# Kernel tuning notes

Measured on AMD Instinct MI355X. Metric: run time of the kernel, lower is better.

Reference implementation:

```python
import jax, jax.numpy as jnp
import numpy as np

N_QUBITS = 7
N_LAYERS = 2
DIM = 2 ** N_QUBITS  # 128
NORM_FACTOR = 1.0


def _cnot_gather_idx(n):
    # CNOT chain (0,1),(1,2),...,(n-2,n-1) plus wraparound (n-1,0).
    # new_state[x] = old_state[idx[x]]; apply gates in reverse to arange.
    gates = [(i, i + 1) for i in range(n - 1)] + [(n - 1, 0)]
    idx = np.arange(2 ** n)
    for c, t in reversed(gates):
        cbit = 1 << (n - 1 - c)  # pennylane wire 0 = most significant bit
        tbit = 1 << (n - 1 - t)
        idx = np.where((idx & cbit) > 0, idx ^ tbit, idx)
    return jnp.asarray(idx)

CNOT_IDX = _cnot_gather_idx(N_QUBITS)


def silu(x):
    return x * jax.nn.sigmoid(x)


def cayley(A_real, A_imag):
    # Hermitianize then Cayley transform -> unitary, per layer. [L,D,D]
    A = A_real.astype(jnp.complex64) + 1j * A_imag.astype(jnp.complex64)
    A = A + jnp.conj(jnp.swapaxes(A, -1, -2))
    I = jnp.eye(DIM, dtype=A.dtype)
    return jnp.matmul(A - 1j * I, jnp.linalg.inv(A + 1j * I))


def _single_qubit_gate(theta_x, theta_y):
    # combined G = RY(theta_y) @ RX(theta_x) applied to every qubit
    cx, sx = jnp.cos(theta_x / 2), jnp.sin(theta_x / 2)
    cy, sy = jnp.cos(theta_y / 2), jnp.sin(theta_y / 2)
    RX = jnp.stack([jnp.stack([cx + 0j, -1j * sx]), jnp.stack([-1j * sx, cx + 0j])])
    RY = jnp.stack([jnp.stack([cy + 0j, -sy + 0j]), jnp.stack([sy + 0j, cy + 0j])])
    return RY @ RX


def quantum_evolve(psi, coeffs, q_mats):
    # psi: [N, DIM] complex64 normalized state vectors
    N = psi.shape[0]
    for j in range(N_LAYERS):
        psi = psi @ q_mats[j].T  # QubitUnitary: new = U @ old
        G = _single_qubit_gate(coeffs[j, 0], coeffs[j, 1])
        psi = psi.reshape((N,) + (2,) * N_QUBITS)
        for ax in range(1, N_QUBITS + 1):
            psi = jnp.moveaxis(jnp.tensordot(G, psi, axes=((1,), (ax,))), 0, ax)
        psi = psi.reshape(N, DIM)
        psi = psi[:, CNOT_IDX]  # CNOT chain is a fixed basis permutation
    return psi


def setup_inputs() -> dict:
    key = jax.random.key(0)
    ks = jax.random.split(key, 16)
    N, E = 50000, 800000
    in_nf, hid, out_nf = 128, 128, 128
    h = jax.random.normal(ks[0], (N, in_nf), dtype=jnp.float32)
    edge_index = jax.random.randint(ks[1], (2, E), 0, N)
    s = 0.05
    W_e1 = jax.random.normal(ks[2], (2 * in_nf, hid), dtype=jnp.float32) * s
    b_e1 = jnp.zeros((hid,), dtype=jnp.float32)
    W_e2 = jax.random.normal(ks[3], (hid, hid), dtype=jnp.float32) * s
    b_e2 = jnp.zeros((hid,), dtype=jnp.float32)
    W_enc = jax.random.normal(ks[4], (hid + in_nf, DIM), dtype=jnp.float32) * s
    b_enc = jnp.zeros((DIM,), dtype=jnp.float32)
    coeffs = jax.random.normal(ks[5], (N_LAYERS, 2), dtype=jnp.float32) * 0.1
    A_real = jax.random.normal(ks[6], (N_LAYERS, DIM, DIM), dtype=jnp.float32) * 0.01
    A_imag = jax.random.normal(ks[7], (N_LAYERS, DIM, DIM), dtype=jnp.float32) * 0.01
    W_dec = jax.random.normal(ks[8], (DIM, out_nf), dtype=jnp.float32) * s
    b_dec = jnp.zeros((out_nf,), dtype=jnp.float32)
    return {"h": h, "edge_index": edge_index, "W_e1": W_e1, "b_e1": b_e1,
            "W_e2": W_e2, "b_e2": b_e2, "W_enc": W_enc, "b_enc": b_enc,
            "coeffs": coeffs, "A_real": A_real, "A_imag": A_imag,
            "W_dec": W_dec, "b_dec": b_dec}


def reference(h, edge_index, W_e1, b_e1, W_e2, b_e2, W_enc, b_enc,
              coeffs, A_real, A_imag, W_dec, b_dec):
    row, col = edge_index[0], edge_index[1]
    # edge model: mij = MLP([h_src, h_tgt])
    e = jnp.concatenate([h[row], h[col]], axis=1)  # [E, 2*in_nf]
    e = silu(e @ W_e1 + b_e1)
    edge_feat = silu(e @ W_e2 + b_e2)  # [E, hid]
    # node model: scatter-sum aggregation over destination `row`
    agg = jax.ops.segment_sum(edge_feat, row, num_segments=h.shape[0]) / NORM_FACTOR
    q_input = jnp.concatenate([h, agg], axis=1) @ W_enc + b_enc  # [N, DIM]
    norm = jnp.sqrt(jnp.sum(q_input ** 2, axis=1, keepdims=True) + 1e-12)
    psi = (q_input / norm).astype(jnp.complex64)
    q_mats = cayley(A_real, A_imag)  # [L, DIM, DIM] unitary
    psi = quantum_evolve(psi, coeffs, q_mats)
    out = h + (jnp.real(psi) @ W_dec + b_dec)
    return out, edge_feat
```

## Files before the change

### kernel.cpp

```cpp
#include <hip/hip_runtime.h>
#include <math.h>

#define N_NODES 50000
#define N_EDGES 800000

typedef __attribute__((ext_vector_type(8))) short bf16x8;
typedef __attribute__((ext_vector_type(4))) short bf16x4;
typedef __attribute__((ext_vector_type(2))) short shortx2;
typedef __attribute__((ext_vector_type(4))) float f32x4;

__device__ __forceinline__ float silu_f(float x) {
    float d = 1.0f + __expf(-x);
    return x * __builtin_amdgcn_rcpf(d);
}

__device__ __forceinline__ unsigned short f2bf(float x) {
    union { float f; unsigned u; } v; v.f = x;
    unsigned r = v.u + 0x7FFFu + ((v.u >> 16) & 1u);
    return (unsigned short)(r >> 16);
}

__device__ __forceinline__ void atomic_pk_add_bf16(short* addr, shortx2 v) {
    typedef shortx2 __attribute__((address_space(1)))* gp1;
    __builtin_amdgcn_global_atomic_fadd_v2bf16((gp1)(unsigned long long)addr, v);
}

__global__ __launch_bounds__(256) void prep_kernel(const float* __restrict__ h,
                                                   short* __restrict__ hbf,
                                                   const int* __restrict__ ei,
                                                   int* __restrict__ cnt,
                                                   const float* __restrict__ A_real,
                                                   const float* __restrict__ A_imag,
                                                   float* __restrict__ H,
                                                   float* __restrict__ X) {
    const int bid = blockIdx.x;
    const int t = threadIdx.x;
    if (bid < 3125) {
        int i = bid * 256 + t;
        const float4* h4 = (const float4*)h;
        float4 v0 = h4[i * 2], v1 = h4[i * 2 + 1];
        bf16x8 b;
        b[0] = (short)f2bf(v0.x); b[1] = (short)f2bf(v0.y);
        b[2] = (short)f2bf(v0.z); b[3] = (short)f2bf(v0.w);
        b[4] = (short)f2bf(v1.x); b[5] = (short)f2bf(v1.y);
        b[6] = (short)f2bf(v1.z); b[7] = (short)f2bf(v1.w);
        ((bf16x8*)hbf)[i] = b;
        atomicAdd(&cnt[ei[i]], 1);
    } else {
        int p = bid - 3125;
        int L = p >> 2, q4 = p & 3;
        const float* ar = A_real + L * 16384;
        const float* ai = A_imag + L * 16384;
        float* hre = H + L * 32768;
        float* him = hre + 16384;
        float* xre = X + L * 32768;
        float* xim = xre + 16384;
        for (int m = 0; m < 16; ++m) {
            int idx = q4 * 4096 + t + 256 * m;
            int i = idx >> 7, j = idx & 127;
            float hr = ar[idx] + ar[j * 128 + i];
            float hi = ai[idx] - ai[j * 128 + i];
            hre[idx] = hr;
            him[idx] = hi;
            xre[idx] = hr;
            xim[idx] = hi - (i == j ? 1.0f : 0.0f);
        }
    }
}

__device__ __forceinline__ void ns_t_body(int blk, int t,
                                          const float* __restrict__ H,
                                          const float* __restrict__ X,
                                          float* __restrict__ T) {
    const int L = blk >> 4;
    const int i = (blk & 15) * 8 + (t >> 7);
    const int j = t & 127;
    const float* hre = H + L * 32768;
    const float* him = hre + 16384;
    const float* xre = X + L * 32768;
    const float* xim = xre + 16384;
    float accr = 0.f, acci = 0.f;
    #pragma unroll 4
    for (int k = 0; k < 128; ++k) {
        float hr = hre[i * 128 + k], hi = him[i * 128 + k];
        float xr = xre[k * 128 + j], xi = xim[k * 128 + j];
        accr += hr * xr - hi * xi;
        acci += hr * xi + hi * xr;
    }
    T[L * 32768 + i * 128 + j]          = accr - xim[i * 128 + j];
    T[L * 32768 + 16384 + i * 128 + j]  = acci + xre[i * 128 + j];
}

__device__ __forceinline__ void ns_x_body(int blk, int t,
                                          const float* __restrict__ X,
                                          const float* __restrict__ T,
                                          float* __restrict__ Xout) {
    const int L = blk >> 4;
    const int i = (blk & 15) * 8 + (t >> 7);
    const int j = t & 127;
    const float* xre = X + L * 32768;
    const float* xim = xre + 16384;
    const float* tre = T + L * 32768;
    const float* tim = tre + 16384;
    float accr = 0.f, acci = 0.f;
    #pragma unroll 4
    for (int k = 0; k < 128; ++k) {
        float xr = xre[i * 128 + k], xi = xim[i * 128 + k];
        float tr = tre[k * 128 + j], ti = tim[k * 128 + j];
        accr += xr * tr - xi * ti;
        acci += xr * ti + xi * tr;
    }
    Xout[L * 32768 + i * 128 + j]          = 2.0f * xre[i * 128 + j] - accr;
    Xout[L * 32768 + 16384 + i * 128 + j]  = 2.0f * xim[i * 128 + j] - acci;
}

__global__ __launch_bounds__(1024) void nst_scan_kernel(const float* __restrict__ H,
                                                        const float* __restrict__ X,
                                                        float* __restrict__ T,
                                                        const int* __restrict__ cnt,
                                                        int* __restrict__ cursor) {
    const int bid = blockIdx.x;
    const int t = threadIdx.x;
    if (bid < 32) { ns_t_body(bid, t, H, X, T); return; }
    __shared__ int sA[1024];
    __shared__ int sB[1024];
    const int CH = 49;
    int s = 0;
    #pragma unroll 4
    for (int i = 0; i < CH; ++i) {
        int idx = t * CH + i;
        if (idx < N_NODES) s += cnt[idx];
    }
    sA[t] = s;
    __syncthreads();
    int* src = sA;
    int* dst = sB;
    for (int off = 1; off < 1024; off <<= 1) {
        int v = src[t];
        if (t >= off) v += src[t - off];
        dst[t] = v;
        __syncthreads();
        int* tmp = src; src = dst; dst = tmp;
    }
    int run = (t == 0) ? 0 : src[t - 1];
    for (int i = 0; i < CH; ++i) {
        int idx = t * CH + i;
        if (idx < N_NODES) {
            cursor[idx] = run;
            run += cnt[idx];
        }
    }
}

__global__ __launch_bounds__(1024) void fill_nsx_kernel(const int* __restrict__ ei,
                                                        int* __restrict__ cursor,
                                                        int* __restrict__ elist,
                                                        const float* __restrict__ X,
                                                        const float* __restrict__ T,
                                                        float* __restrict__ Xout) {
    const int bid = blockIdx.x;
    const int t = threadIdx.x;
    if (bid < 782) {
        int e = bid * 1024 + t;
        if (e < N_EDGES) {
            int slot = atomicAdd(&cursor[ei[e]], 1);
            elist[slot] = e;
        }
        return;
    }
    ns_x_body(bid - 782, t, X, T, Xout);
}

__global__ __launch_bounds__(1024) void ns_t_kernel(const float* __restrict__ H,
                                                    const float* __restrict__ X,
                                                    float* __restrict__ T) {
    ns_t_body(blockIdx.x, threadIdx.x, H, X, T);
}

__global__ __launch_bounds__(1024) void ns_x_kernel(const float* __restrict__ X,
                                                    const float* __restrict__ T,
                                                    float* __restrict__ Xout) {
    ns_x_body(blockIdx.x, threadIdx.x, X, T, Xout);
}

__global__ __launch_bounds__(1024) void gateperm_kernel(const float* __restrict__ X,
                                                        const float* __restrict__ coeffs,
                                                        float* __restrict__ Y) {
    __shared__ float Mre[128 * 129];
    __shared__ float Mim[128 * 129];
    const int L = blockIdx.x;
    const int t = threadIdx.x;
    const float* xre = X + L * 32768;
    const float* xim = xre + 16384;

    for (int q = 0; q < 16; ++q) {
        int idx = t + 1024 * q;
        int i = idx >> 7, j = idx & 127;
        Mre[i * 129 + j] = (i == j ? 1.0f : 0.0f) + 2.0f * xim[idx];
        Mim[i * 129 + j] = -2.0f * xre[idx];
    }
    __syncthreads();

    const float tx = coeffs[2 * L + 0] * 0.5f;
    const float ty = coeffs[2 * L + 1] * 0.5f;
    const float cx = cosf(tx), sx = sinf(tx), cy = cosf(ty), sy = sinf(ty);
    const float G00r = cx * cy, G00i = sx * sy;
    const float G01r = -cx * sy, G01i = -sx * cy;
    const float G10r = cx * sy, G10i = -sx * cy;
    const float G11r = cx * cy, G11i = -sx * sy;

    for (int st = 0; st < 7; ++st) {
        int b = 1 << st;
        #pragma unroll
        for (int p = 0; p < 8; ++p) {
            int pid = t + 1024 * p;
            int col = pid & 127, ph = pid >> 7;
            int i0 = ((ph >> st) << (st + 1)) | (ph & (b - 1));
            int i1 = i0 | b;
            float v0r = Mre[i0 * 129 + col], v0i = Mim[i0 * 129 + col];
            float v1r = Mre[i1 * 129 + col], v1i = Mim[i1 * 129 + col];
            Mre[i0 * 129 + col] = G00r * v0r - G00i * v0i + G01r * v1r - G01i * v1i;
            Mim[i0 * 129 + col] = G00r * v0i + G00i * v0r + G01r * v1i + G01i * v1r;
            Mre[i1 * 129 + col] = G10r * v0r - G10i * v0i + G11r * v1r - G11i * v1i;
            Mim[i1 * 129 + col] = G10r * v0i + G10i * v0r + G11r * v1i + G11i * v1r;
        }
        __syncthreads();
    }

    const int cs[7] = {6, 5, 4, 3, 2, 1, 0};
    const int ts[7] = {0, 6, 5, 4, 3, 2, 1};
    float* yre = Y + L * 32768;
    float* yim = yre + 16384;
    for (int q = 0; q < 16; ++q) {
        int idx = t + 1024 * q;
        int ii_ = idx >> 7, col = idx & 127;
        int s = ii_;
        #pragma unroll
        for (int m = 0; m < 7; ++m) {
            int cbit = 1 << (6 - cs[m]);
            int tbit = 1 << (6 - ts[m]);
            if (s & cbit) s ^= tbit;
        }
        yre[idx] = Mre[s * 129 + col];
        yim[idx] = Mim[s * 129 + col];
    }
}

__global__ __launch_bounds__(512) void combine1_kernel(const float* __restrict__ Y,
                                                       float* __restrict__ ReM) {
    __shared__ float q1r[16384];
    __shared__ float q1i[16384];
    const int t = threadIdx.x;
    const float* q1re = Y;
    const float* q1im = Y + 16384;
    const float* q2re = Y + 32768;
    const float* q2im = Y + 49152;
    for (int q = 0; q < 32; ++q) {
        q1r[t + 512 * q] = q1re[t + 512 * q];
        q1i[t + 512 * q] = q1im[t + 512 * q];
    }
    __syncthreads();
    int i = blockIdx.x * 4 + (t >> 7);
    int j = t & 127;
    float acc = 0.f;
    for (int k = 0; k < 128; ++k) {
        acc += q2re[i * 128 + k] * q1r[k * 128 + j] - q2im[i * 128 + k] * q1i[k * 128 + j];
    }
    ReM[i * 128 + j] = acc;
}

__global__ __launch_bounds__(512) void combine2_kernel(const float* __restrict__ ReM,
                                                       const float* __restrict__ W_dec,
                                                       short* __restrict__ Dt) {
    __shared__ float ml[16384];
    __shared__ float wl[16384];
    const int t = threadIdx.x;
    for (int q = 0; q < 32; ++q) {
        ml[t + 512 * q] = ReM[t + 512 * q];
        wl[t + 512 * q] = W_dec[t + 512 * q];
    }
    __syncthreads();
    int k = blockIdx.x * 4 + (t >> 7);
    int j = t & 127;
    float acc = 0.f;
    for (int i = 0; i < 128; ++i) {
        acc += ml[i * 128 + k] * wl[i * 128 + j];
    }
    Dt[j * 128 + k] = (short)f2bf(acc);
}

__global__ __launch_bounds__(768)
__attribute__((amdgpu_waves_per_eu(3, 3)))
void edge_kernel(const short* __restrict__ hbf,
                 const int* __restrict__ ei,
                 const int* __restrict__ elist,
                 const float* __restrict__ W_e1,
                 const float* __restrict__ b_e1,
                 const float* __restrict__ W_e2,
                 const float* __restrict__ b_e2,
                 float* __restrict__ ef_out,
                 short* __restrict__ agg_bf) {
    __shared__ short w1f[64 * 64 * 8];
    __shared__ short w2f[32 * 64 * 8];
    __shared__ short c1s[12][16 * 68];

    const int t = threadIdx.x;
    const int lane = t & 63;
    const int w = t >> 6;
    const int l15 = lane & 15;
    const int kg = lane >> 4;

    {
        const float4* w1_4 = (const float4*)W_e1;
        for (int idx4 = t; idx4 < 8192; idx4 += 768) {
            int k = idx4 >> 5, j4 = idx4 & 31;
            float4 v = w1_4[idx4];
            int s = k >> 5, kgs = (k >> 3) & 3, e = k & 7;
            int fb = s * 8;
            float vz[4] = {v.x, v.y, v.z, v.w};
            #pragma unroll
            for (int z = 0; z < 4; ++z) {
                int j = j4 * 4 + z;
                int nf = j >> 4, jl = j & 15;
                w1f[((fb + nf) * 64 + kgs * 16 + jl) * 8 + e] = (short)f2bf(vz[z]);
            }
        }
        const float4* w2_4 = (const float4*)W_e2;
        for (int idx4 = t; idx4 < 4096; idx4 += 768) {
            int k = idx4 >> 5, j4 = idx4 & 31;
            float4 v = w2_4[idx4];
            int s2 = k >> 5, kgs = (k >> 3) & 3, e = k & 7;
            int fb = s2 * 8;
            float vz[4] = {v.x, v.y, v.z, v.w};
            #pragma unroll
            for (int z = 0; z < 4; ++z) {
                int j = j4 * 4 + z;
                int nf = j >> 4, jl = j & 15;
                w2f[((fb + nf) * 64 + kgs * 16 + jl) * 8 + e] = (short)f2bf(vz[z]);
            }
        }
    }
    float b1v[8], b2v[8];
    #pragma unroll
    for (int nf = 0; nf < 8; ++nf) {
        b1v[nf] = b_e1[nf * 16 + l15];
        b2v[nf] = b_e2[nf * 16 + l15];
    }
    __syncthreads();

    const bf16x8* hb8 = (const bf16x8*)hbf;
    const bf16x8* w1v = (const bf16x8*)w1f;
    const bf16x8* w2v = (const bf16x8*)w2f;
    short* myc1 = &c1s[w][0];
    const int nt = N_EDGES / 16;
    const int TW = gridDim.x * 12;
    const int wvid = blockIdx.x * 12 + w;
    int tile = (int)(((long long)nt * wvid) / TW);
    const int tend = (int)(((long long)nt * (wvid + 1)) / TW);
    if (tile >= tend) return;

    int el = elist[tile * 16 + l15];
    int ri = ei[el];
    int ci = ei[N_EDGES + el];
    bf16x8 a1[8];
    #pragma unroll
    for (int s = 0; s < 4; ++s) a1[s] = hb8[(size_t)ri * 16 + s * 4 + kg];
    #pragma unroll
    for (int s = 0; s < 4; ++s) a1[4 + s] = hb8[(size_t)ci * 16 + s * 4 + kg];

    bool hn = (tile + 1 < tend);
    int eln = 0, rin = 0, cin = 0;
    if (hn) {
        eln = elist[(tile + 1) * 16 + l15];
        rin = ei[eln];
        cin = ei[N_EDGES + eln];
    }

    float runsum[8];
    #pragma unroll
    for (int nf = 0; nf < 8; ++nf) runsum[nf] = 0.f;

    for (;;) {
        bool hn2 = (tile + 2 < tend);
        int eln2 = 0, rin2 = 0, cin2 = 0;
        if (hn2) {
            eln2 = elist[(tile + 2) * 16 + l15];
            rin2 = ei[eln2];
            cin2 = ei[N_EDGES + eln2];
        }

        f32x4 acc[8];
        #pragma unroll
        for (int nf = 0; nf < 8; ++nf) acc[nf] = (f32x4){0.f, 0.f, 0.f, 0.f};
        #pragma unroll
        for (int s = 0; s < 8; ++s) {
            #pragma unroll
            for (int nf = 0; nf < 8; ++nf) {
                bf16x8 b = w1v[(s * 8 + nf) * 64 + lane];
                acc[nf] = __builtin_amdgcn_mfma_f32_16x16x32_bf16(a1[s], b, acc[nf], 0, 0, 0);
            }
        }

        bf16x8 a1n[8];
        if (hn) {
            #pragma unroll
            for (int s = 0; s < 4; ++s) a1n[s] = hb8[(size_t)rin * 16 + s * 4 + kg];
            #pragma unroll
            for (int s = 0; s < 4; ++s) a1n[4 + s] = hb8[(size_t)cin * 16 + s * 4 + kg];
        }

        f32x4 acc2[8];
        #pragma unroll
        for (int nf = 0; nf < 8; ++nf) acc2[nf] = (f32x4){0.f, 0.f, 0.f, 0.f};
        #pragma unroll
        for (int half = 0; half < 2; ++half) {
            #pragma unroll
            for (int nfh = 0; nfh < 4; ++nfh) {
                int nf = half * 4 + nfh;
                #pragma unroll
                for (int r = 0; r < 4; ++r) {
                    int row = kg * 4 + r;
                    int c = nfh * 16 + l15;
                    myc1[row * 68 + c] = (short)f2bf(silu_f(acc[nf][r] + b1v[nf]));
                }
            }
            #pragma unroll
            for (int s2l = 0; s2l < 2; ++s2l) {
                int k0h = s2l * 32 + kg * 8;
                int base = l15 * 68 + k0h;
                bf16x4 lo = *(const bf16x4*)&myc1[base];
                bf16x4 hi = *(const bf16x4*)&myc1[base + 4];
                bf16x8 a2;
                #pragma unroll
                for (int z = 0; z < 4; ++z) { a2[z] = lo[z]; a2[4 + z] = hi[z]; }
                int s2 = half * 2 + s2l;
                #pragma unroll
                for (int nf = 0; nf < 8; ++nf) {
                    bf16x8 b = w2v[(s2 * 8 + nf) * 64 + lane];
                    acc2[nf] = __builtin_amdgcn_mfma_f32_16x16x32_bf16(a2, b, acc2[nf], 0, 0, 0);
                }
            }
        }

        int rw[4], ew[4];
        #pragma unroll
        for (int r = 0; r < 4; ++r) {
            rw[r] = __shfl(ri, kg * 4 + r);
            ew[r] = __shfl(el, kg * 4 + r);
        }
        int rwn0 = hn ? __shfl(rin, kg * 4) : -1;
        #pragma unroll
        for (int r = 0; r < 4; ++r) {
            float* efp = ef_out + (size_t)ew[r] * 128;
            #pragma unroll
            for (int nf = 0; nf < 8; ++nf) {
                int col = nf * 16 + l15;
                float v = silu_f(acc2[nf][r] + b2v[nf]);
                __builtin_nontemporal_store(v, efp + col);
                runsum[nf] += v;
            }
            bool end = (r < 3) ? (rw[r + 1] != rw[r]) : (rw[3] != rwn0);
            if (end) {
                short* agp = agg_bf + (size_t)rw[r] * 128;
                #pragma unroll
                for (int nf = 0; nf < 8; ++nf) {
                    float vn = __shfl_xor(runsum[nf], 1);
                    if ((l15 & 1) == 0) {
                        shortx2 pk;
                        pk.x = (short)f2bf(runsum[nf]);
                        pk.y = (short)f2bf(vn);
                        atomic_pk_add_bf16(agp + nf * 16 + l15, pk);
                    }
                    runsum[nf] = 0.f;
                }
            }
        }

        if (!hn) break;
        tile += 1;
        el = eln; ri = rin; ci = cin;
        #pragma unroll
        for (int s = 0; s < 8; ++s) a1[s] = a1n[s];
        hn = hn2; eln = eln2; rin = rin2; cin = cin2;
    }
}

__global__ __launch_bounds__(1024)
__attribute__((amdgpu_waves_per_eu(4, 4)))
void node_kernel(const short* __restrict__ hbf,
                 const short* __restrict__ agg_bf,
                 const float* __restrict__ W_enc,
                 const float* __restrict__ b_enc,
                 const short* __restrict__ Dt_bf,
                 const float* __restrict__ b_dec,
                 const float* __restrict__ h,
                 float* __restrict__ out) {
    __shared__ short wef[64 * 64 * 8];
    __shared__ short dtf[32 * 64 * 8];
    __shared__ short c1s[16][16 * 68];

    const int t = threadIdx.x;
    const int lane = t & 63;
    const int w = t >> 6;
    const int l15 = lane & 15;
    const int kg = lane >> 4;

    {
        const float4* we4 = (const float4*)W_enc;
        for (int idx4 = t; idx4 < 8192; idx4 += 1024) {
            int k = idx4 >> 5, j4 = idx4 & 31;
            float4 v = we4[idx4];
            int s = k >> 5, kgs = (k >> 3) & 3, e = k & 7;
            int fb = s * 8;
            float vz[4] = {v.x, v.y, v.z, v.w};
            #pragma unroll
            for (int z = 0; z < 4; ++z) {
                int j = j4 * 4 + z;
                int nf = j >> 4, jl = j & 15;
                wef[((fb + nf) * 64 + kgs * 16 + jl) * 8 + e] = (short)f2bf(vz[z]);
            }
        }
        const bf16x8* dt8 = (const bf16x8*)Dt_bf;
        bf16x8* dtv = (bf16x8*)dtf;
        for (int idx8 = t; idx8 < 2048; idx8 += 1024) {
            int brow = idx8 >> 4, kslot = idx8 & 15;
            int s2 = kslot >> 2, kgs = kslot & 3;
            int nf = brow >> 4, jl = brow & 15;
            dtv[(s2 * 8 + nf) * 64 + kgs * 16 + jl] = dt8[idx8];
        }
    }
    float bj1[8], bj2[8];
    #pragma unroll
    for (int nf = 0; nf < 8; ++nf) {
        bj1[nf] = b_enc[nf * 16 + l15];
        bj2[nf] = b_dec[nf * 16 + l15];
    }
    __syncthreads();

    const bf16x8* hb8 = (const bf16x8*)hbf;
    const bf16x8* ab8 = (const bf16x8*)agg_bf;
    const bf16x8* wev = (const bf16x8*)wef;
    const bf16x8* dtv = (const bf16x8*)dtf;
    short* myc1 = &c1s[w][0];
    const int nt = N_NODES / 16;
    const int tile = blockIdx.x * 16 + w;
    if (tile >= nt) return;

    const int node = tile * 16 + l15;
    bf16x8 a[8];
    #pragma unroll
    for (int s = 0; s < 4; ++s) a[s] = hb8[(size_t)node * 16 + s * 4 + kg];
    #pragma unroll
    for (int s = 0; s < 4; ++s) a[4 + s] = ab8[(size_t)node * 16 + s * 4 + kg];

    f32x4 acc[8];
    #pragma unroll
    for (int nf = 0; nf < 8; ++nf) acc[nf] = (f32x4){0.f, 0.f, 0.f, 0.f};
    #pragma unroll
    for (int s = 0; s < 8; ++s) {
        #pragma unroll
        for (int nf = 0; nf < 8; ++nf) {
            bf16x8 b = wev[(s * 8 + nf) * 64 + lane];
            acc[nf] = __builtin_amdgcn_mfma_f32_16x16x32_bf16(a[s], b, acc[nf], 0, 0, 0);
        }
    }

    float nr[4] = {0.f, 0.f, 0.f, 0.f};
    #pragma unroll
    for (int nf = 0; nf < 8; ++nf) {
        #pragma unroll
        for (int r = 0; r < 4; ++r) {
            acc[nf][r] += bj1[nf];
            nr[r] += acc[nf][r] * acc[nf][r];
        }
    }
    #pragma unroll
    for (int r = 0; r < 4; ++r) {
        nr[r] += __shfl_xor(nr[r], 1);
        nr[r] += __shfl_xor(nr[r], 2);
        nr[r] += __shfl_xor(nr[r], 4);
        nr[r] += __shfl_xor(nr[r], 8);
        nr[r] = 1.0f / sqrtf(nr[r] + 1e-12f);
    }

    f32x4 acc2[8];
    #pragma unroll
    for (int nf = 0; nf < 8; ++nf) acc2[nf] = (f32x4){0.f, 0.f, 0.f, 0.f};
    #pragma unroll
    for (int half = 0; half < 2; ++half) {
        #pragma unroll
        for (int nfh = 0; nfh < 4; ++nfh) {
            int nf = half * 4 + nfh;
            #pragma unroll
            for (int r = 0; r < 4; ++r) {
                int row = kg * 4 + r;
                int c = nfh * 16 + l15;
                myc1[row * 68 + c] = (short)f2bf(acc[nf][r] * nr[r]);
            }
        }
        #pragma unroll
        for (int s2l = 0; s2l < 2; ++s2l) {
            int k0h = s2l * 32 + kg * 8;
            int base = l15 * 68 + k0h;
            bf16x4 lo = *(const bf16x4*)&myc1[base];
            bf16x4 hi = *(const bf16x4*)&myc1[base + 4];
            bf16x8 a2;
            #pragma unroll
            for (int z = 0; z < 4; ++z) { a2[z] = lo[z]; a2[4 + z] = hi[z]; }
            int s2 = half * 2 + s2l;
            #pragma unroll
            for (int nf = 0; nf < 8; ++nf) {
                bf16x8 b = dtv[(s2 * 8 + nf) * 64 + lane];
                acc2[nf] = __builtin_amdgcn_mfma_f32_16x16x32_bf16(a2, b, acc2[nf], 0, 0, 0);
            }
        }
    }

    #pragma unroll
    for (int r = 0; r < 4; ++r) {
        size_t rowb = (size_t)(tile * 16 + kg * 4 + r) * 128;
        #pragma unroll
        for (int nf = 0; nf < 8; ++nf) {
            int col = nf * 16 + l15;
            out[rowb + col] = h[rowb + col] + acc2[nf][r] + bj2[nf];
        }
    }
}

extern "C" void kernel_launch(void* const* d_in, const int* in_sizes, int n_in,
                              void* d_out, int out_size, void* d_ws, size_t ws_size,
                              hipStream_t stream) {
    const float* h      = (const float*)d_in[0];
    const int*   ei     = (const int*)d_in[1];
    const float* W_e1   = (const float*)d_in[2];
    const float* b_e1   = (const float*)d_in[3];
    const float* W_e2   = (const float*)d_in[4];
    const float* b_e2   = (const float*)d_in[5];
    const float* W_enc  = (const float*)d_in[6];
    const float* b_enc  = (const float*)d_in[7];
    const float* coeffs = (const float*)d_in[8];
    const float* A_real = (const float*)d_in[9];
    const float* A_imag = (const float*)d_in[10];
    const float* W_dec  = (const float*)d_in[11];
    const float* b_dec  = (const float*)d_in[12];

    float* out    = (float*)d_out;
    float* ef_out = out + (size_t)N_NODES * 128;

    short* agg_bf = (short*)d_ws;
    int*   cnt    = (int*)(agg_bf + (size_t)N_NODES * 128);
    short* h_bf   = (short*)(cnt + 50176);
    int*   cursor = (int*)(h_bf + (size_t)N_NODES * 128);
    int*   elist  = cursor + 50176;
    float* small  = (float*)(elist + N_EDGES);
    float* Ybuf   = small;
    float* ReM    = Ybuf + 65536;
    float* Hbuf   = ReM + 16384;
    float* Xa     = Hbuf + 65536;
    float* Xb     = Xa + 65536;
    float* Tbuf   = Xb + 65536;
    short* Dt_bf  = (short*)(Tbuf + 65536);

    hipMemsetAsync(agg_bf, 0, (size_t)N_NODES * 128 * sizeof(short) + 50176 * sizeof(int),
                   stream);

    prep_kernel<<<3133, 256, 0, stream>>>(h, h_bf, ei, cnt, A_real, A_imag, Hbuf, Xa);
    nst_scan_kernel<<<33, 1024, 0, stream>>>(Hbuf, Xa, Tbuf, cnt, cursor);
    fill_nsx_kernel<<<814, 1024, 0, stream>>>(ei, cursor, elist, Xa, Tbuf, Xb);
    ns_t_kernel<<<32, 1024, 0, stream>>>(Hbuf, Xb, Tbuf);
    ns_x_kernel<<<32, 1024, 0, stream>>>(Xb, Tbuf, Xa);

    gateperm_kernel<<<2, 1024, 0, stream>>>(Xa, coeffs, Ybuf);
    combine1_kernel<<<32, 512, 0, stream>>>(Ybuf, ReM);
    combine2_kernel<<<32, 512, 0, stream>>>(ReM, W_dec, Dt_bf);

    edge_kernel<<<256, 768, 0, stream>>>(h_bf, ei, elist, W_e1, b_e1, W_e2, b_e2,
                                         ef_out, agg_bf);

    node_kernel<<<196, 1024, 0, stream>>>(h_bf, agg_bf, W_enc, b_enc, Dt_bf, b_dec, h, out);
}
```

Baseline: 593.6 us.

## Fuse small dense-chain kernels into one cooperative kernel and widen edge blocks

Five small kernels (two Newton-Schulz steps, the gate/permutation pass and two combine matmuls) are merged into one cooperative kernel that separates the stages with grid-wide syncs. This is meant to remove launch gaps and tail idle time. The edge kernel also moves from 12 to 16 waves per block with 4 waves per EU, and its next-tile loads now write straight into the a1 registers after the first MFMA stage instead of going through a separate a1n copy, to cut register pressure. The risks are the cost of grid.sync, most blocks sitting idle in the later stages, and lower per-wave register budget in the edge kernel.

```diff
diff --git a/kernel.cpp b/kernel.cpp
--- a/kernel.cpp
+++ b/kernel.cpp
@@ -1,5 +1,8 @@
 #include <hip/hip_runtime.h>
+#include <hip/hip_cooperative_groups.h>
 #include <math.h>
+
+namespace cg = cooperative_groups;
 
 #define N_NODES 50000
 #define N_EDGES 800000
@@ -171,126 +174,126 @@
     ns_x_body(bid - 782, t, X, T, Xout);
 }
 
-__global__ __launch_bounds__(1024) void ns_t_kernel(const float* __restrict__ H,
-                                                    const float* __restrict__ X,
-                                                    float* __restrict__ T) {
-    ns_t_body(blockIdx.x, threadIdx.x, H, X, T);
-}
-
-__global__ __launch_bounds__(1024) void ns_x_kernel(const float* __restrict__ X,
-                                                    const float* __restrict__ T,
-                                                    float* __restrict__ Xout) {
-    ns_x_body(blockIdx.x, threadIdx.x, X, T, Xout);
-}
-
-__global__ __launch_bounds__(1024) void gateperm_kernel(const float* __restrict__ X,
-                                                        const float* __restrict__ coeffs,
-                                                        float* __restrict__ Y) {
-    __shared__ float Mre[128 * 129];
-    __shared__ float Mim[128 * 129];
-    const int L = blockIdx.x;
+__global__ __launch_bounds__(1024) void dchain_kernel(const float* __restrict__ H,
+                                                      const float* __restrict__ Xb,
+                                                      float* __restrict__ T,
+                                                      float* __restrict__ Xa,
+                                                      const float* __restrict__ coeffs,
+                                                      float* __restrict__ Y,
+                                                      float* __restrict__ ReM,
+                                                      const float* __restrict__ W_dec,
+                                                      short* __restrict__ Dt) {
+    cg::grid_group grid = cg::this_grid();
+    __shared__ float smem[128 * 129 * 2];
+    const int bid = blockIdx.x;
     const int t = threadIdx.x;
-    const float* xre = X + L * 32768;
-    const float* xim = xre + 16384;
-
-    for (int q = 0; q < 16; ++q) {
-        int idx = t + 1024 * q;
-        int i = idx >> 7, j = idx & 127;
-        Mre[i * 129 + j] = (i == j ? 1.0f : 0.0f) + 2.0f * xim[idx];
-        Mim[i * 129 + j] = -2.0f * xre[idx];
-    }
-    __syncthreads();
-
-    const float tx = coeffs[2 * L + 0] * 0.5f;
-    const float ty = coeffs[2 * L + 1] * 0.5f;
-    const float cx = cosf(tx), sx = sinf(tx), cy = cosf(ty), sy = sinf(ty);
-    const float G00r = cx * cy, G00i = sx * sy;
-    const float G01r = -cx * sy, G01i = -sx * cy;
-    const float G10r = cx * sy, G10i = -sx * cy;
-    const float G11r = cx * cy, G11i = -sx * sy;
-
-    for (int st = 0; st < 7; ++st) {
-        int b = 1 << st;
-        #pragma unroll
-        for (int p = 0; p < 8; ++p) {
-            int pid = t + 1024 * p;
-            int col = pid & 127, ph = pid >> 7;
-            int i0 = ((ph >> st) << (st + 1)) | (ph & (b - 1));
-            int i1 = i0 | b;
-            float v0r = Mre[i0 * 129 + col], v0i = Mim[i0 * 129 + col];
-            float v1r = Mre[i1 * 129 + col], v1i = Mim[i1 * 129 + col];
-            Mre[i0 * 129 + col] = G00r * v0r - G00i * v0i + G01r * v1r - G01i * v1i;
-            Mim[i0 * 129 + col] = G00r * v0i + G00i * v0r + G01r * v1i + G01i * v1r;
-            Mre[i1 * 129 + col] = G10r * v0r - G10i * v0i + G11r * v1r - G11i * v1i;
-            Mim[i1 * 129 + col] = G10r * v0i + G10i * v0r + G11r * v1i + G11i * v1r;
+
+    ns_t_body(bid, t, H, Xb, T);
+    grid.sync();
+    ns_x_body(bid, t, Xb, T, Xa);
+    grid.sync();
+
+    if (bid < 2) {
+        float* Mre = smem;
+        float* Mim = smem + 128 * 129;
+        const int L = bid;
+        const float* xre = Xa + L * 32768;
+        const float* xim = xre + 16384;
+        for (int q = 0; q < 16; ++q) {
+            int idx = t + 1024 * q;
+            int i = idx >> 7, j = idx & 127;
+            Mre[i * 129 + j] = (i == j ? 1.0f : 0.0f) + 2.0f * xim[idx];
+            Mim[i * 129 + j] = -2.0f * xre[idx];
         }
         __syncthreads();
-    }
-
-    const int cs[7] = {6, 5, 4, 3, 2, 1, 0};
-    const int ts[7] = {0, 6, 5, 4, 3, 2, 1};
-    float* yre = Y + L * 32768;
-    float* yim = yre + 16384;
-    for (int q = 0; q < 16; ++q) {
-        int idx = t + 1024 * q;
-        int ii_ = idx >> 7, col = idx & 127;
-        int s = ii_;
-        #pragma unroll
-        for (int m = 0; m < 7; ++m) {
-            int cbit = 1 << (6 - cs[m]);
-            int tbit = 1 << (6 - ts[m]);
-            if (s & cbit) s ^= tbit;
-        }
-        yre[idx] = Mre[s * 129 + col];
-        yim[idx] = Mim[s * 129 + col];
-    }
-}
-
-__global__ __launch_bounds__(512) void combine1_kernel(const float* __restrict__ Y,
-                                                       float* __restrict__ ReM) {
-    __shared__ float q1r[16384];
-    __shared__ float q1i[16384];
-    const int t = threadIdx.x;
-    const float* q1re = Y;
-    const float* q1im = Y + 16384;
-    const float* q2re = Y + 32768;
-    const float* q2im = Y + 49152;
-    for (int q = 0; q < 32; ++q) {
-        q1r[t + 512 * q] = q1re[t + 512 * q];
-        q1i[t + 512 * q] = q1im[t + 512 * q];
-    }
-    __syncthreads();
-    int i = blockIdx.x * 4 + (t >> 7);
-    int j = t & 127;
-    float acc = 0.f;
-    for (int k = 0; k < 128; ++k) {
-        acc += q2re[i * 128 + k] * q1r[k * 128 + j] - q2im[i * 128 + k] * q1i[k * 128 + j];
-    }
-    ReM[i * 128 + j] = acc;
-}
-
-__global__ __launch_bounds__(512) void combine2_kernel(const float* __restrict__ ReM,
-                                                       const float* __restrict__ W_dec,
-                                                       short* __restrict__ Dt) {
-    __shared__ float ml[16384];
-    __shared__ float wl[16384];
-    const int t = threadIdx.x;
-    for (int q = 0; q < 32; ++q) {
-        ml[t + 512 * q] = ReM[t + 512 * q];
-        wl[t + 512 * q] = W_dec[t + 512 * q];
-    }
-    __syncthreads();
-    int k = blockIdx.x * 4 + (t >> 7);
-    int j = t & 127;
-    float acc = 0.f;
-    for (int i = 0; i < 128; ++i) {
-        acc += ml[i * 128 + k] * wl[i * 128 + j];
-    }
-    Dt[j * 128 + k] = (short)f2bf(acc);
-}
-
-__global__ __launch_bounds__(768)
-__attribute__((amdgpu_waves_per_eu(3, 3)))
+
+        const float tx = coeffs[2 * L + 0] * 0.5f;
+        const float ty = coeffs[2 * L + 1] * 0.5f;
+        const float cx = cosf(tx), sx = sinf(tx), cy = cosf(ty), sy = sinf(ty);
+        const float G00r = cx * cy, G00i = sx * sy;
+        const float G01r = -cx * sy, G01i = -sx * cy;
+        const float G10r = cx * sy, G10i = -sx * cy;
+        const float G11r = cx * cy, G11i = -sx * sy;
+
+        for (int st = 0; st < 7; ++st) {
+            int b = 1 << st;
+            #pragma unroll
+            for (int p = 0; p < 8; ++p) {
+                int pid = t + 1024 * p;
+                int col = pid & 127, ph = pid >> 7;
+                int i0 = ((ph >> st) << (st + 1)) | (ph & (b - 1));
+                int i1 = i0 | b;
+                float v0r = Mre[i0 * 129 + col], v0i = Mim[i0 * 129 + col];
+                float v1r = Mre[i1 * 129 + col], v1i = Mim[i1 * 129 + col];
+                Mre[i0 * 129 + col] = G00r * v0r - G00i * v0i + G01r * v1r - G01i * v1i;
+                Mim[i0 * 129 + col] = G00r * v0i + G00i * v0r + G01r * v1i + G01i * v1r;
+                Mre[i1 * 129 + col] = G10r * v0r - G10i * v0i + G11r * v1r - G11i * v1i;
+                Mim[i1 * 129 + col] = G10r * v0i + G10i * v0r + G11r * v1i + G11i * v1r;
+            }
+            __syncthreads();
+        }
+
+        const int cs[7] = {6, 5, 4, 3, 2, 1, 0};
+        const int ts[7] = {0, 6, 5, 4, 3, 2, 1};
+        float* yre = Y + L * 32768;
+        float* yim = yre + 16384;
+        for (int q = 0; q < 16; ++q) {
+            int idx = t + 1024 * q;
+            int ii_ = idx >> 7, col = idx & 127;
+            int s = ii_;
+            #pragma unroll
+            for (int m = 0; m < 7; ++m) {
+                int cbit = 1 << (6 - cs[m]);
+                int tbit = 1 << (6 - ts[m]);
+                if (s & cbit) s ^= tbit;
+            }
+            yre[idx] = Mre[s * 129 + col];
+            yim[idx] = Mim[s * 129 + col];
+        }
+    }
+    grid.sync();
+
+    if (bid < 16) {
+        float* q1r = smem;
+        float* q1i = smem + 16384;
+        for (int q = 0; q < 16; ++q) {
+            q1r[t + 1024 * q] = Y[t + 1024 * q];
+            q1i[t + 1024 * q] = Y[16384 + t + 1024 * q];
+        }
+        __syncthreads();
+        const float* q2re = Y + 32768;
+        const float* q2im = Y + 49152;
+        int i = bid * 8 + (t >> 7);
+        int j = t & 127;
+        float acc = 0.f;
+        for (int k = 0; k < 128; ++k) {
+            acc += q2re[i * 128 + k] * q1r[k * 128 + j] - q2im[i * 128 + k] * q1i[k * 128 + j];
+        }
+        ReM[i * 128 + j] = acc;
+    }
+    grid.sync();
+
+    if (bid < 16) {
+        float* ml = smem;
+        float* wl = smem + 16384;
+        __syncthreads();
+        for (int q = 0; q < 16; ++q) {
+            ml[t + 1024 * q] = ReM[t + 1024 * q];
+            wl[t + 1024 * q] = W_dec[t + 1024 * q];
+        }
+        __syncthreads();
+        int k = bid * 8 + (t >> 7);
+        int j = t & 127;
+        float acc = 0.f;
+        for (int i = 0; i < 128; ++i) {
+            acc += ml[i * 128 + k] * wl[i * 128 + j];
+        }
+        Dt[j * 128 + k] = (short)f2bf(acc);
+    }
+}
+
+__global__ __launch_bounds__(1024, 4)
+__attribute__((amdgpu_waves_per_eu(4, 4)))
 void edge_kernel(const short* __restrict__ hbf,
                  const int* __restrict__ ei,
                  const int* __restrict__ elist,
@@ -302,7 +305,7 @@
                  short* __restrict__ agg_bf) {
     __shared__ short w1f[64 * 64 * 8];
     __shared__ short w2f[32 * 64 * 8];
-    __shared__ short c1s[12][16 * 68];
+    __shared__ short c1s[16][16 * 68];
 
     const int t = threadIdx.x;
     const int lane = t & 63;
@@ -312,7 +315,7 @@
 
     {
         const float4* w1_4 = (const float4*)W_e1;
-        for (int idx4 = t; idx4 < 8192; idx4 += 768) {
+        for (int idx4 = t; idx4 < 8192; idx4 += 1024) {
             int k = idx4 >> 5, j4 = idx4 & 31;
             float4 v = w1_4[idx4];
             int s = k >> 5, kgs = (k >> 3) & 3, e = k & 7;
@@ -326,7 +329,7 @@
             }
         }
         const float4* w2_4 = (const float4*)W_e2;
-        for (int idx4 = t; idx4 < 4096; idx4 += 768) {
+        for (int idx4 = t; idx4 < 4096; idx4 += 1024) {
             int k = idx4 >> 5, j4 = idx4 & 31;
             float4 v = w2_4[idx4];
             int s2 = k >> 5, kgs = (k >> 3) & 3, e = k & 7;
@@ -353,8 +356,8 @@
     const bf16x8* w2v = (const bf16x8*)w2f;
     short* myc1 = &c1s[w][0];
     const int nt = N_EDGES / 16;
-    const int TW = gridDim.x * 12;
-    const int wvid = blockIdx.x * 12 + w;
+    const int TW = gridDim.x * 16;
+    const int wvid = blockIdx.x * 16 + w;
     int tile = (int)(((long long)nt * wvid) / TW);
     const int tend = (int)(((long long)nt * (wvid + 1)) / TW);
     if (tile >= tend) return;
@@ -381,32 +384,30 @@
     for (int nf = 0; nf < 8; ++nf) runsum[nf] = 0.f;
 
     for (;;) {
+        f32x4 acc[8];
+        #pragma unroll
+        for (int nf = 0; nf < 8; ++nf) acc[nf] = (f32x4){0.f, 0.f, 0.f, 0.f};
+        #pragma unroll
+        for (int s = 0; s < 8; ++s) {
+            #pragma unroll
+            for (int nf = 0; nf < 8; ++nf) {
+                bf16x8 b = w1v[(s * 8 + nf) * 64 + lane];
+                acc[nf] = __builtin_amdgcn_mfma_f32_16x16x32_bf16(a1[s], b, acc[nf], 0, 0, 0);
+            }
+        }
+
+        if (hn) {
+            #pragma unroll
+            for (int s = 0; s < 4; ++s) a1[s] = hb8[(size_t)rin * 16 + s * 4 + kg];
+            #pragma unroll
+            for (int s = 0; s < 4; ++s) a1[4 + s] = hb8[(size_t)cin * 16 + s * 4 + kg];
+        }
         bool hn2 = (tile + 2 < tend);
         int eln2 = 0, rin2 = 0, cin2 = 0;
         if (hn2) {
             eln2 = elist[(tile + 2) * 16 + l15];
             rin2 = ei[eln2];
             cin2 = ei[N_EDGES + eln2];
-        }
-
-        f32x4 acc[8];
-        #pragma unroll
-        for (int nf = 0; nf < 8; ++nf) acc[nf] = (f32x4){0.f, 0.f, 0.f, 0.f};
-        #pragma unroll
-        for (int s = 0; s < 8; ++s) {
-            #pragma unroll
-            for (int nf = 0; nf < 8; ++nf) {
-                bf16x8 b = w1v[(s * 8 + nf) * 64 + lane];
-                acc[nf] = __builtin_amdgcn_mfma_f32_16x16x32_bf16(a1[s], b, acc[nf], 0, 0, 0);
-            }
-        }
-
-        bf16x8 a1n[8];
-        if (hn) {
-            #pragma unroll
-            for (int s = 0; s < 4; ++s) a1n[s] = hb8[(size_t)rin * 16 + s * 4 + kg];
-            #pragma unroll
-            for (int s = 0; s < 4; ++s) a1n[4 + s] = hb8[(size_t)cin * 16 + s * 4 + kg];
         }
 
         f32x4 acc2[8];
@@ -479,8 +480,6 @@
         if (!hn) break;
         tile += 1;
         el = eln; ri = rin; ci = cin;
-        #pragma unroll
-        for (int s = 0; s < 8; ++s) a1[s] = a1n[s];
         hn = hn2; eln = eln2; rin = rin2; cin = cin2;
     }
 }
@@ -667,15 +666,24 @@
     prep_kernel<<<3133, 256, 0, stream>>>(h, h_bf, ei, cnt, A_real, A_imag, Hbuf, Xa);
     nst_scan_kernel<<<33, 1024, 0, stream>>>(Hbuf, Xa, Tbuf, cnt, cursor);
     fill_nsx_kernel<<<814, 1024, 0, stream>>>(ei, cursor, elist, Xa, Tbuf, Xb);
-    ns_t_kernel<<<32, 1024, 0, stream>>>(Hbuf, Xb, Tbuf);
-    ns_x_kernel<<<32, 1024, 0, stream>>>(Xb, Tbuf, Xa);
-
-    gateperm_kernel<<<2, 1024, 0, stream>>>(Xa, coeffs, Ybuf);
-    combine1_kernel<<<32, 512, 0, stream>>>(Ybuf, ReM);
-    combine2_kernel<<<32, 512, 0, stream>>>(ReM, W_dec, Dt_bf);
-
-    edge_kernel<<<256, 768, 0, stream>>>(h_bf, ei, elist, W_e1, b_e1, W_e2, b_e2,
-                                         ef_out, agg_bf);
+
+    {
+        const float* Hc = Hbuf;
+        const float* Xbc = Xb;
+        float* Tc = Tbuf;
+        float* Xac = Xa;
+        const float* cc = coeffs;
+        float* Yc = Ybuf;
+        float* Rc = ReM;
+        const float* Wd = W_dec;
+        short* Dtc = Dt_bf;
+        void* args[] = {&Hc, &Xbc, &Tc, &Xac, &cc, &Yc, &Rc, &Wd, &Dtc};
+        hipLaunchCooperativeKernel((void*)dchain_kernel, dim3(32), dim3(1024),
+                                   args, 0, stream);
+    }
+
+    edge_kernel<<<256, 1024, 0, stream>>>(h_bf, ei, elist, W_e1, b_e1, W_e2, b_e2,
+                                          ef_out, agg_bf);
 
     node_kernel<<<196, 1024, 0, stream>>>(h_bf, agg_bf, W_enc, b_enc, Dt_bf, b_dec, h, out);
 }
```

After: 658.0 us. 1.11x slower.
